# Performance work log

Measured on AMD Instinct MI355X. Metric: run time of the kernel, lower is better.

Reference implementation:

```python
import jax, jax.numpy as jnp
import numpy as np

ANGLE = 0.5  # angular margin from init_kwargs


def setup_inputs() -> dict:
    key = jax.random.key(0)
    k1, k2, k3 = jax.random.split(key, 3)
    B, F, C = 512, 128, 100000
    # scale by 0.1 so exp(features @ w) and exp(modulus * cos) stay finite in fp32
    features = jax.random.normal(k1, (B, F), dtype=jnp.float32) * 0.1
    w = jax.random.normal(k2, (F, C), dtype=jnp.float32) * 0.1
    target = jax.random.randint(k3, (B,), 0, C, dtype=jnp.int64)
    return {"features": features, "w": w, "target": target}


def reference(features, w, target):
    B = features.shape[0]
    rows = jnp.arange(B)
    # norms: [B,1] and [1,C]
    features_modulus = jnp.sqrt(jnp.sum(features ** 2, axis=1, keepdims=True))
    w_modulus = jnp.sqrt(jnp.sum(w ** 2, axis=0, keepdims=True))
    modulus = features_modulus * w_modulus  # [B, C]
    logits = jnp.matmul(features, w)  # [B, C] (computed once; torch computes it twice)
    cos_theta = logits / modulus / 1.01
    theta = jnp.arccos(cos_theta) + ANGLE
    cos_theta_plus = jnp.cos(theta)
    margin_logits = modulus * cos_theta_plus  # [B, C]
    top = jnp.exp(margin_logits[rows, target])  # [B]
    down_ = jnp.exp(logits)  # [B, C]
    down = jnp.sum(down_, axis=1) - down_[rows, target] + top  # [B]
    return -jnp.sum(jnp.log(top / down)) / B
```

## Files before the change

### kernel.cpp

```cpp
#include <hip/hip_runtime.h>

#define F_DIM 128
#define C_DIM 100000
#define B_ROWS 512
#define ANGLE 0.5f
#define CPB 128
#define NCB 782
#define OOB_PAD 96.0f

typedef __attribute__((ext_vector_type(4))) float  f32x4;
typedef __attribute__((ext_vector_type(8))) short  bf16x8;

static __device__ __forceinline__ short f2bf(float x) {
    unsigned int u = __float_as_uint(x);
    u += 0x7FFFu + ((u >> 16) & 1u);
    return (short)(u >> 16);
}

__global__ __launch_bounds__(512, 4)
void arc_main(const float* __restrict__ feat,
              const float* __restrict__ w,
              float* __restrict__ pp)
{
    __shared__ unsigned short lBt[128 * 128];

    const int tid = threadIdx.x;
    const int cb  = blockIdx.x;
    const int c0  = cb * CPB;
    const int r0  = blockIdx.y * 256;

    const int lane = tid & 63;
    const int wv   = tid >> 6;
    const int quad = lane >> 4;
    const int l15  = lane & 15;

    bf16x8 fB[2][4];
    #pragma unroll
    for (int s = 0; s < 2; ++s) {
        const int b = r0 + wv * 32 + s * 16 + l15;
        #pragma unroll
        for (int ks = 0; ks < 4; ++ks) {
            const int k0 = ks * 32 + quad * 8;
            const f32x4 u0 = *(const f32x4*)(feat + b * F_DIM + k0);
            const f32x4 u1 = *(const f32x4*)(feat + b * F_DIM + k0 + 4);
            bf16x8 h;
            h[0] = f2bf(u0[0]); h[1] = f2bf(u0[1]); h[2] = f2bf(u0[2]); h[3] = f2bf(u0[3]);
            h[4] = f2bf(u1[0]); h[5] = f2bf(u1[1]); h[6] = f2bf(u1[2]); h[7] = f2bf(u1[3]);
            fB[s][ks] = h;
        }
    }

    {
        const int c  = tid & 127;
        const int g  = tid >> 7;
        const int gc = c0 + c;
        #pragma unroll
        for (int j = 0; j < 4; ++j) {
            float v[8];
            #pragma unroll
            for (int i = 0; i < 8; ++i) {
                const int k = g * 32 + j * 8 + i;
                v[i] = (gc < C_DIM) ? w[(size_t)k * C_DIM + gc] : 0.f;
            }
            bf16x8 h;
            #pragma unroll
            for (int i = 0; i < 8; ++i) h[i] = f2bf(v[i]);
            const int pc = (g * 4 + j) ^ (c & 15);
            *(bf16x8*)&lBt[c * 128 + pc * 8] = h;
        }
    }
    __syncthreads();

    float eA0 = 0.f, eA1 = 0.f, eA2 = 0.f, eA3 = 0.f;
    float eB0 = 0.f, eB1 = 0.f, eB2 = 0.f, eB3 = 0.f;
    #pragma unroll
    for (int m = 0; m < 8; ++m) {
        f32x4 a0 = {0.f, 0.f, 0.f, 0.f};
        f32x4 a1 = {0.f, 0.f, 0.f, 0.f};
        const int row = m * 16 + l15;
        #pragma unroll
        for (int ks = 0; ks < 4; ++ks) {
            const int pc = (ks * 4 + quad) ^ (row & 15);
            const bf16x8 af = *(const bf16x8*)&lBt[row * 128 + pc * 8];
            a0 = __builtin_amdgcn_mfma_f32_16x16x32_bf16(af, fB[0][ks], a0, 0, 0, 0);
            a1 = __builtin_amdgcn_mfma_f32_16x16x32_bf16(af, fB[1][ks], a1, 0, 0, 0);
        }
        eA0 += __expf(a0[0]); eA1 += __expf(a0[1]);
        eA2 += __expf(a0[2]); eA3 += __expf(a0[3]);
        eB0 += __expf(a1[0]); eB1 += __expf(a1[1]);
        eB2 += __expf(a1[2]); eB3 += __expf(a1[3]);
    }

    float esum0 = (eA0 + eA1) + (eA2 + eA3);
    float esum1 = (eB0 + eB1) + (eB2 + eB3);
    esum0 += __shfl_xor(esum0, 16); esum0 += __shfl_xor(esum0, 32);
    esum1 += __shfl_xor(esum1, 16); esum1 += __shfl_xor(esum1, 32);
    if (lane < 16) {
        pp[(size_t)cb * 512 + r0 + wv * 32 + lane]      = esum0;
        pp[(size_t)cb * 512 + r0 + wv * 32 + 16 + lane] = esum1;
    }
}

__global__ void arc_row(const float* __restrict__ feat,
                        const float* __restrict__ w,
                        const int*   __restrict__ target,
                        const float* __restrict__ pp,
                        float* __restrict__ term)
{
    const int b    = blockIdx.x;
    const int lane = threadIdx.x;
    const int t    = target[b];

    float dot = 0.f, wsq = 0.f, fsq = 0.f, rs = 0.f;
    #pragma unroll
    for (int h = 0; h < 2; ++h) {
        const int f  = lane + h * 64;
        const float fv = feat[b * F_DIM + f];
        const float wv = w[(size_t)f * C_DIM + t];
        dot += fv * wv;
        wsq += wv * wv;
        fsq += fv * fv;
    }
    for (int j = lane; j < NCB; j += 64)
        rs += pp[(size_t)j * 512 + b];

    #pragma unroll
    for (int off = 32; off > 0; off >>= 1) {
        dot += __shfl_xor(dot, off);
        wsq += __shfl_xor(wsq, off);
        fsq += __shfl_xor(fsq, off);
        rs  += __shfl_xor(rs,  off);
    }
    if (lane == 0) {
        const float mod = sqrtf(fsq) * sqrtf(wsq);
        float ct = dot / (mod * 1.01f);
        ct = fminf(1.f, fmaxf(-1.f, ct));
        const float th   = acosf(ct) + ANGLE;
        const float marg = mod * cosf(th);
        const float down = rs - OOB_PAD - expf(dot) + expf(marg);
        term[b] = marg - logf(down);
    }
}

__global__ void arc_loss(const float* __restrict__ term,
                         float* __restrict__ out)
{
    __shared__ float red[B_ROWS];
    const int b = threadIdx.x;
    red[b] = term[b];
    __syncthreads();
    #pragma unroll
    for (int st = 256; st > 0; st >>= 1) {
        if (b < st) red[b] += red[b + st];
        __syncthreads();
    }
    if (b == 0) out[0] = -red[0] / (float)B_ROWS;
}

extern "C" void kernel_launch(void* const* d_in, const int* in_sizes, int n_in,
                              void* d_out, int out_size, void* d_ws, size_t ws_size,
                              hipStream_t stream)
{
    const float* feat   = (const float*)d_in[0];
    const float* w      = (const float*)d_in[1];
    const int*   target = (const int*)d_in[2];

    float* pp   = (float*)d_ws;
    float* term = pp + (size_t)NCB * 512;

    arc_main<<<dim3(NCB, 2), 512, 0, stream>>>(feat, w, pp);
    arc_row<<<B_ROWS, 64, 0, stream>>>(feat, w, target, pp, term);
    arc_loss<<<1, B_ROWS, 0, stream>>>(term, (float*)d_out);
}
```

Before: 131.4 us.

## Pre-transpose W to bf16 in a separate pass and read MFMA operands from global memory

Adds a kernel that converts W to bf16 and transposes it into a padded class-major buffer once per call. The main MFMA kernel then loads operands straight from that buffer instead of staging fp32 W through swizzled shared memory, which drops the LDS tile and its barrier. The row kernel now uses the bf16 transposed target weights, and both the row and final reductions are restructured to use fewer, wider blocks. In exchange there is an extra launch and a full write and reread of a half-size copy of W, and the target-column dot product now uses bf16 rather than fp32 weights.

```diff
diff --git a/kernel.cpp b/kernel.cpp
--- a/kernel.cpp
+++ b/kernel.cpp
@@ -6,6 +6,7 @@
 #define ANGLE 0.5f
 #define CPB 128
 #define NCB 782
+#define CPAD 100096
 #define OOB_PAD 96.0f
 
 typedef __attribute__((ext_vector_type(4))) float  f32x4;
@@ -16,19 +17,43 @@
     u += 0x7FFFu + ((u >> 16) & 1u);
     return (short)(u >> 16);
 }
+static __device__ __forceinline__ float bf2f(unsigned short u) {
+    return __uint_as_float((unsigned int)u << 16);
+}
+
+__global__ __launch_bounds__(256)
+void arc_tr(const float* __restrict__ w, unsigned short* __restrict__ w_t)
+{
+    const int tid = threadIdx.x;
+    const int cl  = tid & 63;
+    const int kh  = tid >> 6;
+    const int c   = blockIdx.x * 64 + cl;
+
+    bf16x8 h[4];
+    if (c < C_DIM) {
+        #pragma unroll
+        for (int q = 0; q < 4; ++q)
+            #pragma unroll
+            for (int i = 0; i < 8; ++i)
+                h[q][i] = f2bf(w[(size_t)(kh * 32 + q * 8 + i) * C_DIM + c]);
+    } else {
+        #pragma unroll
+        for (int q = 0; q < 4; ++q)
+            h[q] = (bf16x8){0, 0, 0, 0, 0, 0, 0, 0};
+    }
+    #pragma unroll
+    for (int q = 0; q < 4; ++q)
+        *(bf16x8*)&w_t[(size_t)c * 128 + kh * 32 + q * 8] = h[q];
+}
 
 __global__ __launch_bounds__(512, 4)
 void arc_main(const float* __restrict__ feat,
-              const float* __restrict__ w,
+              const unsigned short* __restrict__ w_t,
               float* __restrict__ pp)
 {
-    __shared__ unsigned short lBt[128 * 128];
-
-    const int tid = threadIdx.x;
-    const int cb  = blockIdx.x;
-    const int c0  = cb * CPB;
-    const int r0  = blockIdx.y * 256;
-
+    const int tid  = threadIdx.x;
+    const int c0   = blockIdx.x * CPB;
+    const int r0   = blockIdx.y * 256;
     const int lane = tid & 63;
     const int wv   = tid >> 6;
     const int quad = lane >> 4;
@@ -50,38 +75,16 @@
         }
     }
 
-    {
-        const int c  = tid & 127;
-        const int g  = tid >> 7;
-        const int gc = c0 + c;
-        #pragma unroll
-        for (int j = 0; j < 4; ++j) {
-            float v[8];
-            #pragma unroll
-            for (int i = 0; i < 8; ++i) {
-                const int k = g * 32 + j * 8 + i;
-                v[i] = (gc < C_DIM) ? w[(size_t)k * C_DIM + gc] : 0.f;
-            }
-            bf16x8 h;
-            #pragma unroll
-            for (int i = 0; i < 8; ++i) h[i] = f2bf(v[i]);
-            const int pc = (g * 4 + j) ^ (c & 15);
-            *(bf16x8*)&lBt[c * 128 + pc * 8] = h;
-        }
-    }
-    __syncthreads();
-
     float eA0 = 0.f, eA1 = 0.f, eA2 = 0.f, eA3 = 0.f;
     float eB0 = 0.f, eB1 = 0.f, eB2 = 0.f, eB3 = 0.f;
     #pragma unroll
     for (int m = 0; m < 8; ++m) {
+        const unsigned short* wr = w_t + (size_t)(c0 + m * 16 + l15) * 128 + quad * 8;
         f32x4 a0 = {0.f, 0.f, 0.f, 0.f};
         f32x4 a1 = {0.f, 0.f, 0.f, 0.f};
-        const int row = m * 16 + l15;
         #pragma unroll
         for (int ks = 0; ks < 4; ++ks) {
-            const int pc = (ks * 4 + quad) ^ (row & 15);
-            const bf16x8 af = *(const bf16x8*)&lBt[row * 128 + pc * 8];
+            const bf16x8 af = *(const bf16x8*)(wr + ks * 32);
             a0 = __builtin_amdgcn_mfma_f32_16x16x32_bf16(af, fB[0][ks], a0, 0, 0, 0);
             a1 = __builtin_amdgcn_mfma_f32_16x16x32_bf16(af, fB[1][ks], a1, 0, 0, 0);
         }
@@ -96,65 +99,87 @@
     esum0 += __shfl_xor(esum0, 16); esum0 += __shfl_xor(esum0, 32);
     esum1 += __shfl_xor(esum1, 16); esum1 += __shfl_xor(esum1, 32);
     if (lane < 16) {
-        pp[(size_t)cb * 512 + r0 + wv * 32 + lane]      = esum0;
-        pp[(size_t)cb * 512 + r0 + wv * 32 + 16 + lane] = esum1;
-    }
-}
-
-__global__ void arc_row(const float* __restrict__ feat,
-                        const float* __restrict__ w,
-                        const int*   __restrict__ target,
-                        const float* __restrict__ pp,
-                        float* __restrict__ term)
-{
-    const int b    = blockIdx.x;
-    const int lane = threadIdx.x;
-    const int t    = target[b];
-
-    float dot = 0.f, wsq = 0.f, fsq = 0.f, rs = 0.f;
-    #pragma unroll
-    for (int h = 0; h < 2; ++h) {
-        const int f  = lane + h * 64;
-        const float fv = feat[b * F_DIM + f];
-        const float wv = w[(size_t)f * C_DIM + t];
-        dot += fv * wv;
-        wsq += wv * wv;
-        fsq += fv * fv;
-    }
-    for (int j = lane; j < NCB; j += 64)
-        rs += pp[(size_t)j * 512 + b];
-
-    #pragma unroll
-    for (int off = 32; off > 0; off >>= 1) {
-        dot += __shfl_xor(dot, off);
-        wsq += __shfl_xor(wsq, off);
-        fsq += __shfl_xor(fsq, off);
-        rs  += __shfl_xor(rs,  off);
-    }
-    if (lane == 0) {
-        const float mod = sqrtf(fsq) * sqrtf(wsq);
-        float ct = dot / (mod * 1.01f);
+        pp[(size_t)blockIdx.x * 512 + r0 + wv * 32 + lane]      = esum0;
+        pp[(size_t)blockIdx.x * 512 + r0 + wv * 32 + 16 + lane] = esum1;
+    }
+}
+
+__global__ __launch_bounds__(256)
+void arc_row(const float* __restrict__ feat,
+             const unsigned short* __restrict__ w_t,
+             const int* __restrict__ target,
+             const float* __restrict__ pp,
+             float* __restrict__ pl)
+{
+    __shared__ float sPP[4][64];
+    __shared__ float sDot[4][64];
+    __shared__ float sFsq[4][64];
+    __shared__ float sWsq[4][64];
+    __shared__ float sT[64];
+
+    const int tid = threadIdx.x;
+    const int bl  = tid & 63;
+    const int gr  = tid >> 6;
+    const int b   = blockIdx.x * 64 + bl;
+
+    float acc = 0.f;
+    for (int j = gr; j < NCB; j += 4)
+        acc += pp[(size_t)j * 512 + b];
+    sPP[gr][bl] = acc;
+
+    const int tg = target[b];
+    const unsigned short* wr = w_t + (size_t)tg * 128 + gr * 32;
+    const float*          fr = feat + b * F_DIM + gr * 32;
+    float dot = 0.f, fsq = 0.f, wsq = 0.f;
+    #pragma unroll
+    for (int i = 0; i < 4; ++i) {
+        const bf16x8 hw = *(const bf16x8*)(wr + i * 8);
+        const f32x4  f0 = *(const f32x4*)(fr + i * 8);
+        const f32x4  f1 = *(const f32x4*)(fr + i * 8 + 4);
+        #pragma unroll
+        for (int j = 0; j < 4; ++j) {
+            const float wv0 = bf2f((unsigned short)hw[j]);
+            const float wv1 = bf2f((unsigned short)hw[j + 4]);
+            dot += f0[j] * wv0 + f1[j] * wv1;
+            wsq += wv0 * wv0 + wv1 * wv1;
+            fsq += f0[j] * f0[j] + f1[j] * f1[j];
+        }
+    }
+    sDot[gr][bl] = dot; sFsq[gr][bl] = fsq; sWsq[gr][bl] = wsq;
+    __syncthreads();
+
+    if (tid < 64) {
+        const int r = tid;
+        const float d  = sDot[0][r] + sDot[1][r] + sDot[2][r] + sDot[3][r];
+        const float fq = sFsq[0][r] + sFsq[1][r] + sFsq[2][r] + sFsq[3][r];
+        const float wq = sWsq[0][r] + sWsq[1][r] + sWsq[2][r] + sWsq[3][r];
+        const float rs = sPP[0][r] + sPP[1][r] + sPP[2][r] + sPP[3][r] - OOB_PAD;
+        const float mod = sqrtf(fq) * sqrtf(wq);
+        float ct = d / (mod * 1.01f);
         ct = fminf(1.f, fmaxf(-1.f, ct));
         const float th   = acosf(ct) + ANGLE;
         const float marg = mod * cosf(th);
-        const float down = rs - OOB_PAD - expf(dot) + expf(marg);
-        term[b] = marg - logf(down);
-    }
-}
-
-__global__ void arc_loss(const float* __restrict__ term,
-                         float* __restrict__ out)
-{
-    __shared__ float red[B_ROWS];
-    const int b = threadIdx.x;
-    red[b] = term[b];
+        const float down = rs - expf(d) + expf(marg);
+        sT[r] = marg - logf(down);
+    }
     __syncthreads();
-    #pragma unroll
-    for (int st = 256; st > 0; st >>= 1) {
-        if (b < st) red[b] += red[b + st];
-        __syncthreads();
-    }
-    if (b == 0) out[0] = -red[0] / (float)B_ROWS;
+
+    if (tid < 32) sT[tid] += sT[tid + 32];
+    __syncthreads();
+    if (tid < 64) {
+        float v = (tid < 32) ? sT[tid] : 0.f;
+        #pragma unroll
+        for (int off = 16; off > 0; off >>= 1)
+            v += __shfl_xor(v, off);
+        if (tid == 0) pl[blockIdx.x] = v;
+    }
+}
+
+__global__ void arc_loss(const float* __restrict__ pl, float* __restrict__ out)
+{
+    float v = (threadIdx.x < 8) ? pl[threadIdx.x] : 0.f;
+    v += __shfl_xor(v, 1); v += __shfl_xor(v, 2); v += __shfl_xor(v, 4);
+    if (threadIdx.x == 0) out[0] = -v / (float)B_ROWS;
 }
 
 extern "C" void kernel_launch(void* const* d_in, const int* in_sizes, int n_in,
@@ -165,10 +190,12 @@
     const float* w      = (const float*)d_in[1];
     const int*   target = (const int*)d_in[2];
 
-    float* pp   = (float*)d_ws;
-    float* term = pp + (size_t)NCB * 512;
-
-    arc_main<<<dim3(NCB, 2), 512, 0, stream>>>(feat, w, pp);
-    arc_row<<<B_ROWS, 64, 0, stream>>>(feat, w, target, pp, term);
-    arc_loss<<<1, B_ROWS, 0, stream>>>(term, (float*)d_out);
-}
+    unsigned short* w_t = (unsigned short*)d_ws;
+    float* pp = (float*)(w_t + (size_t)CPAD * 128);
+    float* pl = pp + (size_t)NCB * 512;
+
+    arc_tr  <<<CPAD / 64, 256, 0, stream>>>(w, w_t);
+    arc_main<<<dim3(NCB, 2), 512, 0, stream>>>(feat, w_t, pp);
+    arc_row <<<8, 256, 0, stream>>>(feat, w_t, target, pp, pl);
+    arc_loss<<<1, 64, 0, stream>>>(pl, (float*)d_out);
+}
```

Result: slower. 222.8 us (+69.6%).

## Process all rows per block and pre-convert features to scaled bf16

Applied to the files above, without the earlier changes.

Drops the grid's second dimension so each block handles all 512 rows for its 128 columns, loading and converting the w tile to bf16 once instead of twice. A new prep kernel converts features to bf16 once, pre-scaled by log2(e), so the main loop can use the hardware exp2 in place of __expf. The bf16 conversion now uses the packed library intrinsic. In exchange, each wave holds four times the fragment and accumulator registers, which may lower occupancy under the launch bounds, and there is one extra kernel launch.

```diff
diff --git a/kernel.cpp b/kernel.cpp
--- a/kernel.cpp
+++ b/kernel.cpp
@@ -1,4 +1,5 @@
 #include <hip/hip_runtime.h>
+#include <hip/hip_bf16.h>
 
 #define F_DIM 128
 #define C_DIM 100000
@@ -11,14 +12,34 @@
 typedef __attribute__((ext_vector_type(4))) float  f32x4;
 typedef __attribute__((ext_vector_type(8))) short  bf16x8;
 
-static __device__ __forceinline__ short f2bf(float x) {
-    unsigned int u = __float_as_uint(x);
-    u += 0x7FFFu + ((u >> 16) & 1u);
-    return (short)(u >> 16);
+static __device__ __forceinline__ unsigned int pk2(float a, float b) {
+    __hip_bfloat162 h = __float22bfloat162_rn(float2{a, b});
+    return *(unsigned int*)&h;
+}
+
+#if __has_builtin(__builtin_amdgcn_exp2f)
+#define EXP2(x) __builtin_amdgcn_exp2f(x)
+#else
+#define EXP2(x) exp2f(x)
+#endif
+
+__global__ __launch_bounds__(256)
+void arc_prep(const float* __restrict__ feat, unsigned short* __restrict__ fbf)
+{
+    const int i = (blockIdx.x * 256 + threadIdx.x) * 8;
+    const float s = 1.4426950408889634f;
+    const f32x4 a = *(const f32x4*)(feat + i);
+    const f32x4 b = *(const f32x4*)(feat + i + 4);
+    union { bf16x8 h; unsigned int u[4]; } fr;
+    fr.u[0] = pk2(a[0] * s, a[1] * s);
+    fr.u[1] = pk2(a[2] * s, a[3] * s);
+    fr.u[2] = pk2(b[0] * s, b[1] * s);
+    fr.u[3] = pk2(b[2] * s, b[3] * s);
+    *(bf16x8*)&fbf[i] = fr.h;
 }
 
 __global__ __launch_bounds__(512, 4)
-void arc_main(const float* __restrict__ feat,
+void arc_main(const unsigned short* __restrict__ fbf,
               const float* __restrict__ w,
               float* __restrict__ pp)
 {
@@ -27,28 +48,6 @@
     const int tid = threadIdx.x;
     const int cb  = blockIdx.x;
     const int c0  = cb * CPB;
-    const int r0  = blockIdx.y * 256;
-
-    const int lane = tid & 63;
-    const int wv   = tid >> 6;
-    const int quad = lane >> 4;
-    const int l15  = lane & 15;
-
-    bf16x8 fB[2][4];
-    #pragma unroll
-    for (int s = 0; s < 2; ++s) {
-        const int b = r0 + wv * 32 + s * 16 + l15;
-        #pragma unroll
-        for (int ks = 0; ks < 4; ++ks) {
-            const int k0 = ks * 32 + quad * 8;
-            const f32x4 u0 = *(const f32x4*)(feat + b * F_DIM + k0);
-            const f32x4 u1 = *(const f32x4*)(feat + b * F_DIM + k0 + 4);
-            bf16x8 h;
-            h[0] = f2bf(u0[0]); h[1] = f2bf(u0[1]); h[2] = f2bf(u0[2]); h[3] = f2bf(u0[3]);
-            h[4] = f2bf(u1[0]); h[5] = f2bf(u1[1]); h[6] = f2bf(u1[2]); h[7] = f2bf(u1[3]);
-            fB[s][ks] = h;
-        }
-    }
 
     {
         const int c  = tid & 127;
@@ -62,42 +61,62 @@
                 const int k = g * 32 + j * 8 + i;
                 v[i] = (gc < C_DIM) ? w[(size_t)k * C_DIM + gc] : 0.f;
             }
-            bf16x8 h;
-            #pragma unroll
-            for (int i = 0; i < 8; ++i) h[i] = f2bf(v[i]);
+            union { bf16x8 h; unsigned int u[4]; } fr;
+            fr.u[0] = pk2(v[0], v[1]); fr.u[1] = pk2(v[2], v[3]);
+            fr.u[2] = pk2(v[4], v[5]); fr.u[3] = pk2(v[6], v[7]);
             const int pc = (g * 4 + j) ^ (c & 15);
-            *(bf16x8*)&lBt[c * 128 + pc * 8] = h;
+            *(bf16x8*)&lBt[c * 128 + pc * 8] = fr.h;
         }
+    }
+
+    const int lane = tid & 63;
+    const int wv   = tid >> 6;
+    const int quad = lane >> 4;
+    const int l15  = lane & 15;
+
+    bf16x8 fB[4][4];
+    #pragma unroll
+    for (int s = 0; s < 4; ++s) {
+        const unsigned short* fr = fbf + (size_t)(wv * 64 + s * 16 + l15) * F_DIM + quad * 8;
+        #pragma unroll
+        for (int ks = 0; ks < 4; ++ks)
+            fB[s][ks] = *(const bf16x8*)(fr + ks * 32);
     }
     __syncthreads();
 
-    float eA0 = 0.f, eA1 = 0.f, eA2 = 0.f, eA3 = 0.f;
-    float eB0 = 0.f, eB1 = 0.f, eB2 = 0.f, eB3 = 0.f;
+    float esum[4][4];
+    #pragma unroll
+    for (int s = 0; s < 4; ++s)
+        #pragma unroll
+        for (int r = 0; r < 4; ++r) esum[s][r] = 0.f;
+
     #pragma unroll
     for (int m = 0; m < 8; ++m) {
-        f32x4 a0 = {0.f, 0.f, 0.f, 0.f};
-        f32x4 a1 = {0.f, 0.f, 0.f, 0.f};
         const int row = m * 16 + l15;
+        f32x4 acc[4];
+        #pragma unroll
+        for (int s = 0; s < 4; ++s) acc[s] = (f32x4){0.f, 0.f, 0.f, 0.f};
         #pragma unroll
         for (int ks = 0; ks < 4; ++ks) {
             const int pc = (ks * 4 + quad) ^ (row & 15);
             const bf16x8 af = *(const bf16x8*)&lBt[row * 128 + pc * 8];
-            a0 = __builtin_amdgcn_mfma_f32_16x16x32_bf16(af, fB[0][ks], a0, 0, 0, 0);
-            a1 = __builtin_amdgcn_mfma_f32_16x16x32_bf16(af, fB[1][ks], a1, 0, 0, 0);
+            #pragma unroll
+            for (int s = 0; s < 4; ++s)
+                acc[s] = __builtin_amdgcn_mfma_f32_16x16x32_bf16(af, fB[s][ks], acc[s], 0, 0, 0);
         }
-        eA0 += __expf(a0[0]); eA1 += __expf(a0[1]);
-        eA2 += __expf(a0[2]); eA3 += __expf(a0[3]);
-        eB0 += __expf(a1[0]); eB1 += __expf(a1[1]);
-        eB2 += __expf(a1[2]); eB3 += __expf(a1[3]);
+        #pragma unroll
+        for (int s = 0; s < 4; ++s) {
+            esum[s][0] += EXP2(acc[s][0]); esum[s][1] += EXP2(acc[s][1]);
+            esum[s][2] += EXP2(acc[s][2]); esum[s][3] += EXP2(acc[s][3]);
+        }
     }
 
-    float esum0 = (eA0 + eA1) + (eA2 + eA3);
-    float esum1 = (eB0 + eB1) + (eB2 + eB3);
-    esum0 += __shfl_xor(esum0, 16); esum0 += __shfl_xor(esum0, 32);
-    esum1 += __shfl_xor(esum1, 16); esum1 += __shfl_xor(esum1, 32);
-    if (lane < 16) {
-        pp[(size_t)cb * 512 + r0 + wv * 32 + lane]      = esum0;
-        pp[(size_t)cb * 512 + r0 + wv * 32 + 16 + lane] = esum1;
+    #pragma unroll
+    for (int s = 0; s < 4; ++s) {
+        float e = (esum[s][0] + esum[s][1]) + (esum[s][2] + esum[s][3]);
+        e += __shfl_xor(e, 16); e += __shfl_xor(e, 32);
+        if (lane < 16)
+            pp[(size_t)cb * 512 + wv * 64 + s * 16 + lane] = e;
     }
 }
 
@@ -165,10 +184,12 @@
     const float* w      = (const float*)d_in[1];
     const int*   target = (const int*)d_in[2];
 
-    float* pp   = (float*)d_ws;
+    unsigned short* fbf = (unsigned short*)d_ws;
+    float* pp   = (float*)(fbf + (size_t)B_ROWS * F_DIM);
     float* term = pp + (size_t)NCB * 512;
 
-    arc_main<<<dim3(NCB, 2), 512, 0, stream>>>(feat, w, pp);
-    arc_row<<<B_ROWS, 64, 0, stream>>>(feat, w, target, pp, term);
+    arc_prep<<<32, 256, 0, stream>>>(feat, fbf);
+    arc_main<<<NCB, 512, 0, stream>>>(fbf, w, pp);
+    arc_row <<<B_ROWS, 64, 0, stream>>>(feat, w, target, pp, term);
     arc_loss<<<1, B_ROWS, 0, stream>>>(term, (float*)d_out);
 }
```

Result: slower. 166.5 us (+26.8%).
